# Performance work log

Hardware: AMD Instinct MI355X
Metric: run time of the kernel (lower is better)

## Reference

```python
import jax, jax.numpy as jnp
import numpy as np

B, N, F, D, DEG, LAYERS = 32, 1024, 64, 128, 8, 3
EPS = 1e-5


def _gat(x, src, dst, mask, W, a_s, a_d, b):
    # PyG GATConv (heads=1, concat=True): remove existing self loops (handled by mask),
    # add one self loop per node, per-edge leaky-relu attention, scatter-softmax per target.
    M = x.shape[0]
    h = x @ W                                 # [M, D]
    es = h @ a_s                              # [M] source attention term (x*att_src).sum(-1)
    ed = h @ a_d                              # [M] target attention term
    sl = jnp.arange(M, dtype=src.dtype)
    s = jnp.concatenate([src, sl])
    d = jnp.concatenate([dst, sl])
    m = jnp.concatenate([mask, jnp.ones((M,), bool)])
    logit = jnp.where(m, jax.nn.leaky_relu(es[s] + ed[d], 0.2), -jnp.inf)
    mx = jax.ops.segment_max(logit, d, num_segments=M)  # finite: every node has a self loop
    ex = jnp.where(m, jnp.exp(logit - mx[d]), 0.0)
    den = jax.ops.segment_sum(ex, d, num_segments=M)
    alpha = ex / den[d]
    return jax.ops.segment_sum(alpha[:, None] * h[s], d, num_segments=M) + b


def _dedupe(src, dst, mask, M):
    # coalesce after pooling: drop self loops and duplicate edges (PyG max_pool/pool_edge)
    E = src.shape[0]
    key = src * M + dst
    key = jnp.where(mask, key, M * M + jnp.arange(E, dtype=key.dtype))  # park dead edges on unique keys
    order = jnp.argsort(key)
    sk = key[order]
    first = jnp.concatenate([jnp.ones((1,), bool), sk[1:] != sk[:-1]])
    uniq = jnp.zeros((E,), bool).at[order].set(first)
    return mask & uniq & (src != dst)


def _forward(x, Ws, att_src, att_dst, bias, edge_index, clusters):
    src, dst = edge_index[0], edge_index[1]
    mask = src != dst  # GATConv calls remove_self_loops before adding its own
    Bn = x.shape[0] // clusters[0].shape[0]
    for i in range(len(Ws)):
        x = jax.nn.relu(_gat(x, src, dst, mask, Ws[i], att_src[i], att_dst[i], bias[i]))
        c = clusters[i]
        Ni = c.shape[0]
        No = Ni // 2  # cluster maps are arange(Ni)//2, surjective onto Ni//2
        cl = jnp.tile(c, Bn) + jnp.repeat(jnp.arange(Bn, dtype=c.dtype) * No, Ni)
        x = jax.ops.segment_max(x, cl, num_segments=Bn * No)  # max_pool over clusters
        src, dst = cl[src], cl[dst]
        mask = _dedupe(src, dst, mask, Bn * No)
        mu = jnp.mean(x, axis=0)  # BatchNorm1d(affine=False), training-mode batch stats
        var = jnp.mean((x - mu) ** 2, axis=0)
        x = (x - mu) / jnp.sqrt(var + EPS)
    return x.reshape(Bn, -1)  # [B, final_node * dim_cell]


def setup_inputs() -> dict:
    key = jax.random.key(0)
    ks = jax.random.split(key, 10)
    x = jax.random.normal(ks[0], (B * N, F), jnp.float32)
    # per-graph random edges with per-graph node offsets (graph-major layout)
    src_l = jax.random.randint(ks[1], (B, N * DEG), 0, N)
    dst_l = jax.random.randint(ks[2], (B, N * DEG), 0, N)
    off = (jnp.arange(B) * N)[:, None]
    edge_index = jnp.stack([(src_l + off).reshape(-1), (dst_l + off).reshape(-1)]).astype(jnp.int32)
    c0 = (jnp.arange(N) // 2).astype(jnp.int32)
    c1 = (jnp.arange(N // 2) // 2).astype(jnp.int32)
    c2 = (jnp.arange(N // 4) // 2).astype(jnp.int32)
    W0 = jax.random.normal(ks[3], (F, D), jnp.float32) / np.float32(np.sqrt(F))
    W1 = jax.random.normal(ks[4], (D, D), jnp.float32) / np.float32(np.sqrt(D))
    W2 = jax.random.normal(ks[5], (D, D), jnp.float32) / np.float32(np.sqrt(D))
    att_src = jax.random.normal(ks[6], (LAYERS, D), jnp.float32) / np.float32(np.sqrt(D))
    att_dst = jax.random.normal(ks[7], (LAYERS, D), jnp.float32) / np.float32(np.sqrt(D))
    bias = jnp.zeros((LAYERS, D), jnp.float32)
    return dict(x=x, W0=W0, W1=W1, W2=W2, att_src=att_src, att_dst=att_dst, bias=bias,
                edge_index=edge_index, c0=c0, c1=c1, c2=c2)


def reference(x, W0, W1, W2, att_src, att_dst, bias, edge_index, c0, c1, c2):
    return _forward(x, [W0, W1, W2], att_src, att_dst, bias, edge_index, [c0, c1, c2])
```

## Files before the change

### kernel.cpp

```cpp
#include <hip/hip_runtime.h>

#define E_TOTAL 262144
#define NGRAPH  32
#define EPG     8192
#define EPS_BN  1e-5f
#define MB (1u << 20)
#define KB (1u << 10)

__device__ __forceinline__ float lrelu(float x){ return x > 0.f ? x : 0.2f * x; }

__device__ __forceinline__ int xcd_swz(int b, int n){ return (b & 7) * (n >> 3) + (b >> 3); }

template<int K>
__global__ __launch_bounds__(256)
void gemm_attn(const float* __restrict__ A, const float* __restrict__ W,
               const float* __restrict__ bnsums, float invM,
               const float* __restrict__ a_s, const float* __restrict__ a_d,
               float* __restrict__ C, float* __restrict__ es, float* __restrict__ ed){
  __shared__ float Ws[64 * 128];
  __shared__ float As_t[64 * 36];
  __shared__ float bnmu[K], bnrs[K];
  int tid = threadIdx.x;
  if (tid < K){
    float mu = 0.f, rs = 1.f;
    if (bnsums){
      mu = bnsums[tid] * invM;
      float var = bnsums[K + tid] * invM - mu * mu;
      rs = rsqrtf(var + EPS_BN);
    }
    bnmu[tid] = mu; bnrs[tid] = rs;
  }
  int bid = xcd_swz(blockIdx.x, gridDim.x);
  int row0 = bid * 32;
  int c2 = tid & 63, rg = tid >> 6;
  float2 acc[8];
  #pragma unroll
  for (int i = 0; i < 8; ++i){ acc[i].x = 0.f; acc[i].y = 0.f; }

  for (int k0 = 0; k0 < K; k0 += 64){
    __syncthreads();
    for (int i = tid; i < 64 * 128; i += 256)
      Ws[i] = W[(size_t)(k0 + (i >> 7)) * 128 + (i & 127)];
    #pragma unroll
    for (int it = 0; it < 8; ++it){
      int i = it * 256 + tid;
      int r = i >> 6, kk = i & 63;
      float v = A[(size_t)(row0 + r) * K + k0 + kk];
      v = (v - bnmu[k0 + kk]) * bnrs[k0 + kk];
      As_t[kk * 36 + r] = v;
    }
    __syncthreads();
    #pragma unroll 8
    for (int kk = 0; kk < 64; ++kk){
      float2 w = *(float2*)&Ws[kk * 128 + c2 * 2];
      float4 a0 = *(float4*)&As_t[kk * 36 + rg * 8];
      float4 a1 = *(float4*)&As_t[kk * 36 + rg * 8 + 4];
      acc[0].x = fmaf(a0.x, w.x, acc[0].x); acc[0].y = fmaf(a0.x, w.y, acc[0].y);
      acc[1].x = fmaf(a0.y, w.x, acc[1].x); acc[1].y = fmaf(a0.y, w.y, acc[1].y);
      acc[2].x = fmaf(a0.z, w.x, acc[2].x); acc[2].y = fmaf(a0.z, w.y, acc[2].y);
      acc[3].x = fmaf(a0.w, w.x, acc[3].x); acc[3].y = fmaf(a0.w, w.y, acc[3].y);
      acc[4].x = fmaf(a1.x, w.x, acc[4].x); acc[4].y = fmaf(a1.x, w.y, acc[4].y);
      acc[5].x = fmaf(a1.y, w.x, acc[5].x); acc[5].y = fmaf(a1.y, w.y, acc[5].y);
      acc[6].x = fmaf(a1.z, w.x, acc[6].x); acc[6].y = fmaf(a1.z, w.y, acc[6].y);
      acc[7].x = fmaf(a1.w, w.x, acc[7].x); acc[7].y = fmaf(a1.w, w.y, acc[7].y);
    }
  }
  float2 as2 = ((const float2*)a_s)[c2];
  float2 ad2 = ((const float2*)a_d)[c2];
  float2* C2 = (float2*)C;
  #pragma unroll
  for (int i = 0; i < 8; ++i){
    int r = row0 + rg * 8 + i;
    C2[(size_t)r * 64 + c2] = acc[i];
    float e1 = acc[i].x * as2.x + acc[i].y * as2.y;
    float e2 = acc[i].x * ad2.x + acc[i].y * ad2.y;
    #pragma unroll
    for (int o = 32; o; o >>= 1){ e1 += __shfl_xor(e1, o); e2 += __shfl_xor(e2, o); }
    if (c2 == 0){ es[r] = e1; ed[r] = e2; }
  }
}

__global__ __launch_bounds__(1024)
void csr_build_all(const int* __restrict__ src0, const int* __restrict__ dst0,
                   int* __restrict__ csr1, int* __restrict__ csr2, int* __restrict__ csr3,
                   int* __restrict__ rs1, int* __restrict__ rs2, int* __restrict__ rs3,
                   int* __restrict__ cnt1, int* __restrict__ cnt2, int* __restrict__ cnt3,
                   float* __restrict__ bnsums){
  __shared__ unsigned int bm2[8192];
  __shared__ unsigned int bm3[2048];
  __shared__ int h1[1024];
  __shared__ int h2[512];
  __shared__ int h3[256];
  __shared__ int wsum[16];
  int g = blockIdx.x, t = threadIdx.x;
  int ebase = g * EPG;
  if (g == 0 && t < 768) bnsums[t] = 0.f;
  #pragma unroll
  for (int i = t; i < 8192; i += 1024) bm2[i] = 0u;
  #pragma unroll
  for (int i = t; i < 2048; i += 1024) bm3[i] = 0u;
  h1[t] = 0;
  if (t < 512) h2[t] = 0;
  if (t < 256) h3[t] = 0;
  __syncthreads();

  unsigned int k1 = 0, k2 = 0, k3 = 0;
  #pragma unroll
  for (int k = 0; k < 8; ++k){
    int e = ebase + k * 1024 + t;
    int sv = src0[e], dv = dst0[e];
    if (sv != dv){
      k1 |= 1u << k;
      atomicAdd(&h1[dv & 1023], 1);
      int s2 = (sv >> 1) & 511, d2 = (dv >> 1) & 511;
      if (s2 != d2){
        int key = (s2 << 9) | d2;
        unsigned int bit = 1u << (key & 31);
        unsigned int old = atomicOr(&bm2[key >> 5], bit);
        if (!(old & bit)){
          k2 |= 1u << k;
          atomicAdd(&h2[d2], 1);
          int s3 = (sv >> 2) & 255, d3 = (dv >> 2) & 255;
          if (s3 != d3){
            int key3 = (s3 << 8) | d3;
            unsigned int b3 = 1u << (key3 & 31);
            unsigned int o3 = atomicOr(&bm3[key3 >> 5], b3);
            if (!(o3 & b3)){ k3 |= 1u << k; atomicAdd(&h3[d3], 1); }
          }
        }
      }
    }
  }
  __syncthreads();

  int lane = t & 63, w = t >> 6;
  {
    int c = h1[t], v = c;
    #pragma unroll
    for (int o = 1; o < 64; o <<= 1){ int u = __shfl_up(v, o); if (lane >= o) v += u; }
    if (lane == 63) wsum[w] = v;
    __syncthreads();
    if (t == 0){ int run = 0;
      #pragma unroll
      for (int i = 0; i < 16; ++i){ int x = wsum[i]; wsum[i] = run; run += x; } }
    __syncthreads();
    int excl = v - c + wsum[w];
    cnt1[(g << 10) + t] = c;
    rs1 [(g << 10) + t] = ebase + excl;
    h1[t] = excl;
  }
  __syncthreads();
  {
    int c = (t < 512) ? h2[t] : 0, v = c;
    #pragma unroll
    for (int o = 1; o < 64; o <<= 1){ int u = __shfl_up(v, o); if (lane >= o) v += u; }
    if (lane == 63) wsum[w] = v;
    __syncthreads();
    if (t == 0){ int run = 0;
      #pragma unroll
      for (int i = 0; i < 16; ++i){ int x = wsum[i]; wsum[i] = run; run += x; } }
    __syncthreads();
    int excl = v - c + wsum[w];
    if (t < 512){
      cnt2[(g << 9) + t] = c;
      rs2 [(g << 9) + t] = ebase + excl;
      h2[t] = excl;
    }
  }
  __syncthreads();
  {
    int c = (t < 256) ? h3[t] : 0, v = c;
    #pragma unroll
    for (int o = 1; o < 64; o <<= 1){ int u = __shfl_up(v, o); if (lane >= o) v += u; }
    if (lane == 63) wsum[w] = v;
    __syncthreads();
    if (t == 0){ int run = 0;
      #pragma unroll
      for (int i = 0; i < 16; ++i){ int x = wsum[i]; wsum[i] = run; run += x; } }
    __syncthreads();
    int excl = v - c + wsum[w];
    if (t < 256){
      cnt3[(g << 8) + t] = c;
      rs3 [(g << 8) + t] = ebase + excl;
      h3[t] = excl;
    }
  }
  __syncthreads();

  unsigned int any = k1 | k2 | k3;
  #pragma unroll
  for (int k = 0; k < 8; ++k){
    if ((any >> k) & 1u){
      int e = ebase + k * 1024 + t;
      int sv = src0[e], dv = dst0[e];
      if ((k1 >> k) & 1u){
        int p = atomicAdd(&h1[dv & 1023], 1);
        csr1[ebase + p] = sv;
      }
      if ((k2 >> k) & 1u){
        int p = atomicAdd(&h2[(dv >> 1) & 511], 1);
        csr2[ebase + p] = sv >> 1;
      }
      if ((k3 >> k) & 1u){
        int p = atomicAdd(&h3[(dv >> 2) & 255], 1);
        csr3[ebase + p] = sv >> 2;
      }
    }
  }
}

__global__ void gat_pool(const float* __restrict__ h, const float* __restrict__ es,
                         const float* __restrict__ ed, const int* __restrict__ csr_src,
                         const int* __restrict__ row_start, const int* __restrict__ row_cnt,
                         const float* __restrict__ bias, float* __restrict__ xout, int M){
  __shared__ float2 osh[4][64];
  int lane = threadIdx.x & 63;
  int wave = threadIdx.x >> 6;
  int bid = xcd_swz(blockIdx.x, gridDim.x);
  int n = bid * 4 + wave;
  int start = row_start[n];
  int cnt   = row_cnt[n];
  float edn = ed[n];
  float selfl = lrelu(es[n] + edn);

  float m_l = -1e30f, d_l = 0.f;
  int   s_c = 0; float l_c = 0.f;
  for (int c0 = 0; c0 < cnt; c0 += 64){
    int j = c0 + lane;
    if (j < cnt){
      int s = csr_src[start + j];
      float l = lrelu(es[s] + edn);
      if (c0 == 0){ s_c = s; l_c = l; }
      float mn = fmaxf(m_l, l);
      d_l = d_l * __expf(m_l - mn) + __expf(l - mn);
      m_l = mn;
    }
  }
  #pragma unroll
  for (int o = 32; o; o >>= 1){
    float m2 = __shfl_xor(m_l, o), d2 = __shfl_xor(d_l, o);
    float mn = fmaxf(m_l, m2);
    d_l = d_l * __expf(m_l - mn) + d2 * __expf(m2 - mn);
    m_l = mn;
  }
  float mf  = fmaxf(m_l, selfl);
  float den = d_l * __expf(m_l - mf) + __expf(selfl - mf);

  const float2* h2 = (const float2*)h;
  float sw = __expf(selfl - mf);
  float2 hv = h2[(size_t)n * 64 + lane];
  float2 acc; acc.x = sw * hv.x; acc.y = sw * hv.y;
  for (int c0 = 0; c0 < cnt; c0 += 64){
    int j = c0 + lane;
    int s_j; float w_j;
    if (c0 == 0){
      s_j = s_c;
      w_j = (lane < cnt) ? __expf(l_c - mf) : 0.f;
    } else {
      s_j = 0; w_j = 0.f;
      if (j < cnt){
        s_j = csr_src[start + j];
        w_j = __expf(lrelu(es[s_j] + edn) - mf);
      }
    }
    int rem = min(64, cnt - c0);
    int k = 0;
    for (; k + 8 <= rem; k += 8){
      int ss[8]; float ww[8]; float2 hh[8];
      #pragma unroll
      for (int i = 0; i < 8; ++i){ ss[i] = __shfl(s_j, k + i); ww[i] = __shfl(w_j, k + i); }
      #pragma unroll
      for (int i = 0; i < 8; ++i){ hh[i] = h2[(size_t)ss[i] * 64 + lane]; }
      #pragma unroll
      for (int i = 0; i < 8; ++i){
        acc.x = fmaf(ww[i], hh[i].x, acc.x);
        acc.y = fmaf(ww[i], hh[i].y, acc.y);
      }
    }
    for (; k < rem; ++k){
      int s = __shfl(s_j, k); float w = __shfl(w_j, k);
      float2 hh = h2[(size_t)s * 64 + lane];
      acc.x = fmaf(w, hh.x, acc.x);
      acc.y = fmaf(w, hh.y, acc.y);
    }
  }
  float inv = 1.f / den;
  float2 bv = ((const float2*)bias)[lane];
  float2 o2;
  o2.x = fmaxf(acc.x * inv + bv.x, 0.f);
  o2.y = fmaxf(acc.y * inv + bv.y, 0.f);
  osh[wave][lane] = o2;
  __syncthreads();
  if (wave < 2){
    float2 a = osh[2 * wave][lane], b = osh[2 * wave + 1][lane];
    float2 p; p.x = fmaxf(a.x, b.x); p.y = fmaxf(a.y, b.y);
    ((float2*)xout)[(size_t)(bid * 2 + wave) * 64 + lane] = p;
  }
}

__global__ void bn_stats(const float* __restrict__ x, float* __restrict__ sums, int M){
  __shared__ float s1[256], s2[256];
  int c = threadIdx.x & 127, half = threadIdx.x >> 7;
  float a = 0.f, b = 0.f;
  for (int r = blockIdx.x * 2 + half; r < M; r += 256){
    float v = x[(size_t)r * 128 + c];
    a += v; b += v * v;
  }
  s1[threadIdx.x] = a; s2[threadIdx.x] = b;
  __syncthreads();
  if (threadIdx.x < 128){
    atomicAdd(&sums[c],       s1[threadIdx.x] + s1[threadIdx.x + 128]);
    atomicAdd(&sums[128 + c], s2[threadIdx.x] + s2[threadIdx.x + 128]);
  }
}

__global__ void bn_norm(const float* __restrict__ in, const float* __restrict__ sums,
                        float* __restrict__ out, int M){
  int idx = blockIdx.x * blockDim.x + threadIdx.x;
  if (idx >= M * 128) return;
  int c = idx & 127;
  float mu  = sums[c] / (float)M;
  float var = sums[128 + c] / (float)M - mu * mu;
  out[idx] = (in[idx] - mu) * rsqrtf(var + EPS_BN);
}

extern "C" void kernel_launch(void* const* d_in, const int* in_sizes, int n_in,
                              void* d_out, int out_size, void* d_ws, size_t ws_size,
                              hipStream_t stream){
  const float* x0   = (const float*)d_in[0];
  const float* W0   = (const float*)d_in[1];
  const float* W1   = (const float*)d_in[2];
  const float* W2   = (const float*)d_in[3];
  const float* attS = (const float*)d_in[4];
  const float* attD = (const float*)d_in[5];
  const float* bias = (const float*)d_in[6];
  const int*   src0 = (const int*)d_in[7];
  const int*   dst0 = src0 + E_TOTAL;
  float* out = (float*)d_out;

  char* ws = (char*)d_ws;
  float* Hbuf   = (float*)(ws);
  float* Xbuf   = (float*)(ws + 16 * MB);
  int*   csr1   = (int*)  (ws + 24 * MB);
  int*   csr2   = (int*)  (ws + 25 * MB);
  int*   csr3   = (int*)  (ws + 26 * MB);
  float* es     = (float*)(ws + 27 * MB);
  float* ed     = (float*)(ws + 27 * MB + 128 * KB);
  int*   rs1    = (int*)  (ws + 27 * MB + 256 * KB);
  int*   rs2    = (int*)  (ws + 27 * MB + 384 * KB);
  int*   rs3    = (int*)  (ws + 27 * MB + 448 * KB);
  int*   cnt1   = (int*)  (ws + 27 * MB + 480 * KB);
  int*   cnt2   = (int*)  (ws + 27 * MB + 608 * KB);
  int*   cnt3   = (int*)  (ws + 27 * MB + 672 * KB);
  float* bnsum0 = (float*)(ws + 27 * MB + 704 * KB);
  float* bnsum1 = bnsum0 + 256;
  float* bnsum2 = bnsum1 + 256;

  csr_build_all<<<NGRAPH, 1024, 0, stream>>>(src0, dst0, csr1, csr2, csr3,
                                             rs1, rs2, rs3, cnt1, cnt2, cnt3, bnsum0);

  gemm_attn<64><<<1024, 256, 0, stream>>>(x0, W0, nullptr, 0.f, attS, attD, Hbuf, es, ed);
  gat_pool<<<8192, 256, 0, stream>>>(Hbuf, es, ed, csr1, rs1, cnt1, bias, Xbuf, 32768);
  bn_stats<<<128, 256, 0, stream>>>(Xbuf, bnsum0, 16384);

  gemm_attn<128><<<512, 256, 0, stream>>>(Xbuf, W1, bnsum0, 1.f / 16384.f,
                                          attS + 128, attD + 128, Hbuf, es, ed);
  gat_pool<<<4096, 256, 0, stream>>>(Hbuf, es, ed, csr2, rs2, cnt2, bias + 128, Xbuf, 16384);
  bn_stats<<<128, 256, 0, stream>>>(Xbuf, bnsum1, 8192);

  gemm_attn<128><<<256, 256, 0, stream>>>(Xbuf, W2, bnsum1, 1.f / 8192.f,
                                          attS + 256, attD + 256, Hbuf, es, ed);
  gat_pool<<<2048, 256, 0, stream>>>(Hbuf, es, ed, csr3, rs3, cnt3, bias + 256, Xbuf, 8192);
  bn_stats<<<128, 256, 0, stream>>>(Xbuf, bnsum2, 4096);
  bn_norm<<<2048, 256, 0, stream>>>(Xbuf, bnsum2, out, 4096);
}
```

Before: 240.7 us.

## Fuse CSR build with first GEMM and fold BN stats into grid-barrier kernels

Merges the per-graph CSR construction into the first GEMM launch. 96 extra blocks split the three CSR levels across separate blocks, so edge preprocessing runs alongside the layer-0 matmul. The BN statistics passes are folded into the following GEMM and final-normalise kernels behind a software grid barrier, which removes several launches. The barrier assumes every block is co-resident (512 blocks at 256 threads with launch bounds of 2 per CU) and risks deadlock or spin overhead. The level-3 CSR block also redoes the level-2 dedupe on its own.

```diff
diff --git a/kernel.cpp b/kernel.cpp
--- a/kernel.cpp
+++ b/kernel.cpp
@@ -11,41 +11,249 @@
 
 __device__ __forceinline__ int xcd_swz(int b, int n){ return (b & 7) * (n >> 3) + (b >> 3); }
 
-template<int K>
-__global__ __launch_bounds__(256)
-void gemm_attn(const float* __restrict__ A, const float* __restrict__ W,
-               const float* __restrict__ bnsums, float invM,
-               const float* __restrict__ a_s, const float* __restrict__ a_d,
-               float* __restrict__ C, float* __restrict__ es, float* __restrict__ ed){
+__device__ __forceinline__ void grid_bar(int* bar, int n){
+  __syncthreads();
+  if (threadIdx.x == 0){
+    __hip_atomic_fetch_add(bar, 1, __ATOMIC_RELEASE, __HIP_MEMORY_SCOPE_AGENT);
+    while (__hip_atomic_load(bar, __ATOMIC_RELAXED, __HIP_MEMORY_SCOPE_AGENT) < n)
+      __builtin_amdgcn_s_sleep(8);
+    (void)__hip_atomic_load(bar, __ATOMIC_ACQUIRE, __HIP_MEMORY_SCOPE_AGENT);
+  }
+  __syncthreads();
+}
+
+template<int Q>
+__device__ __forceinline__ void scan_bins(int* h, int* cnt_g, int* rs_g, int B, int g,
+                                          int ebase, int* wsum){
+  int t = threadIdx.x, lane = t & 63, w = t >> 6;
+  int c[Q]; int s = 0;
+  #pragma unroll
+  for (int i = 0; i < Q; ++i){ c[i] = h[t * Q + i]; s += c[i]; }
+  int v = s;
+  #pragma unroll
+  for (int o = 1; o < 64; o <<= 1){ int u = __shfl_up(v, o); if (lane >= o) v += u; }
+  if (lane == 63) wsum[w] = v;
+  __syncthreads();
+  if (t == 0){ int run = 0;
+    #pragma unroll
+    for (int i = 0; i < 4; ++i){ int x = wsum[i]; wsum[i] = run; run += x; } }
+  __syncthreads();
+  int run = v - s + wsum[w];
+  #pragma unroll
+  for (int i = 0; i < Q; ++i){
+    cnt_g[g * B + t * Q + i] = c[i];
+    rs_g [g * B + t * Q + i] = ebase + run;
+    h[t * Q + i] = run;
+    run += c[i];
+  }
+  __syncthreads();
+}
+
+__global__ __launch_bounds__(256, 2)
+void mega1(const float* __restrict__ x0, const float* __restrict__ W0,
+           const float* __restrict__ a_s, const float* __restrict__ a_d,
+           const int* __restrict__ src0, const int* __restrict__ dst0,
+           float* __restrict__ C, float* __restrict__ es, float* __restrict__ ed,
+           int* __restrict__ csr1, int* __restrict__ csr2, int* __restrict__ csr3,
+           int* __restrict__ rs1, int* __restrict__ rs2, int* __restrict__ rs3,
+           int* __restrict__ cnt1, int* __restrict__ cnt2, int* __restrict__ cnt3,
+           float* __restrict__ sums_all, int* __restrict__ bars){
+  __shared__ __align__(16) char smem[45072];
+  __shared__ int wsum[4];
+  int t = threadIdx.x;
+  int raw = blockIdx.x;
+
+  if (raw < 96){
+    int* bm2 = (int*)smem;
+    int* bm3 = bm2 + 8192;
+    int* h   = bm3 + 2048;
+    int role = raw >> 5, g = raw & 31, ebase = g * EPG;
+    if (raw == 0 && t < 48) bars[t] = 0;
+    if (role == 0 && t < 24) sums_all[g * 24 + t] = 0.f;
+
+    if (role == 0){
+      for (int i = t; i < 1024; i += 256) h[i] = 0;
+      __syncthreads();
+      for (int i = 0; i < 32; ++i){
+        int e = ebase + i * 256 + t;
+        int sv = src0[e], dv = dst0[e];
+        if (sv != dv) atomicAdd(&h[dv & 1023], 1);
+      }
+      __syncthreads();
+      scan_bins<4>(h, cnt1, rs1, 1024, g, ebase, wsum);
+      for (int i = 0; i < 32; ++i){
+        int e = ebase + i * 256 + t;
+        int sv = src0[e], dv = dst0[e];
+        if (sv != dv){
+          int p = atomicAdd(&h[dv & 1023], 1);
+          csr1[ebase + p] = sv;
+        }
+      }
+    } else if (role == 1){
+      for (int i = t; i < 8192; i += 256) bm2[i] = 0;
+      for (int i = t; i < 512; i += 256) h[i] = 0;
+      __syncthreads();
+      unsigned int k2m = 0;
+      for (int i = 0; i < 32; ++i){
+        int e = ebase + i * 256 + t;
+        int sv = src0[e], dv = dst0[e];
+        if (sv != dv){
+          int s2 = (sv >> 1) & 511, d2 = (dv >> 1) & 511;
+          if (s2 != d2){
+            int key = (s2 << 9) | d2;
+            unsigned int bit = 1u << (key & 31);
+            unsigned int old = atomicOr((unsigned int*)&bm2[key >> 5], bit);
+            if (!(old & bit)){ k2m |= 1u << i; atomicAdd(&h[d2], 1); }
+          }
+        }
+      }
+      __syncthreads();
+      scan_bins<2>(h, cnt2, rs2, 512, g, ebase, wsum);
+      for (int i = 0; i < 32; ++i){
+        if ((k2m >> i) & 1u){
+          int e = ebase + i * 256 + t;
+          int sv = src0[e], dv = dst0[e];
+          int p = atomicAdd(&h[(dv >> 1) & 511], 1);
+          csr2[ebase + p] = sv >> 1;
+        }
+      }
+    } else {
+      for (int i = t; i < 8192; i += 256) bm2[i] = 0;
+      for (int i = t; i < 2048; i += 256) bm3[i] = 0;
+      for (int i = t; i < 256; i += 256) h[i] = 0;
+      __syncthreads();
+      unsigned int k3m = 0;
+      for (int i = 0; i < 32; ++i){
+        int e = ebase + i * 256 + t;
+        int sv = src0[e], dv = dst0[e];
+        if (sv != dv){
+          int s2 = (sv >> 1) & 511, d2 = (dv >> 1) & 511;
+          if (s2 != d2){
+            int key = (s2 << 9) | d2;
+            unsigned int bit = 1u << (key & 31);
+            unsigned int old = atomicOr((unsigned int*)&bm2[key >> 5], bit);
+            if (!(old & bit)){
+              int s3 = (sv >> 2) & 255, d3 = (dv >> 2) & 255;
+              if (s3 != d3){
+                int key3 = (s3 << 8) | d3;
+                unsigned int b3 = 1u << (key3 & 31);
+                unsigned int o3 = atomicOr((unsigned int*)&bm3[key3 >> 5], b3);
+                if (!(o3 & b3)){ k3m |= 1u << i; atomicAdd(&h[d3], 1); }
+              }
+            }
+          }
+        }
+      }
+      __syncthreads();
+      scan_bins<1>(h, cnt3, rs3, 256, g, ebase, wsum);
+      for (int i = 0; i < 32; ++i){
+        if ((k3m >> i) & 1u){
+          int e = ebase + i * 256 + t;
+          int sv = src0[e], dv = dst0[e];
+          int p = atomicAdd(&h[(dv >> 2) & 255], 1);
+          csr3[ebase + p] = sv >> 2;
+        }
+      }
+    }
+    return;
+  }
+
+  float* Ws   = (float*)smem;
+  float* As_t = Ws + 8192;
+  int tile = xcd_swz(raw - 96, 1024);
+  int row0 = tile * 32;
+  int c2 = t & 63, rg = t >> 6;
+  float2 acc[8];
+  #pragma unroll
+  for (int i = 0; i < 8; ++i){ acc[i].x = 0.f; acc[i].y = 0.f; }
+
+  for (int i = t; i < 8192; i += 256) Ws[i] = W0[i];
+  #pragma unroll
+  for (int it = 0; it < 8; ++it){
+    int i = it * 256 + t;
+    int r = i >> 6, kk = i & 63;
+    As_t[kk * 36 + r] = x0[(size_t)(row0 + r) * 64 + kk];
+  }
+  __syncthreads();
+  #pragma unroll 8
+  for (int kk = 0; kk < 64; ++kk){
+    float2 w = *(float2*)&Ws[kk * 128 + c2 * 2];
+    float4 a0 = *(float4*)&As_t[kk * 36 + rg * 8];
+    float4 a1 = *(float4*)&As_t[kk * 36 + rg * 8 + 4];
+    acc[0].x = fmaf(a0.x, w.x, acc[0].x); acc[0].y = fmaf(a0.x, w.y, acc[0].y);
+    acc[1].x = fmaf(a0.y, w.x, acc[1].x); acc[1].y = fmaf(a0.y, w.y, acc[1].y);
+    acc[2].x = fmaf(a0.z, w.x, acc[2].x); acc[2].y = fmaf(a0.z, w.y, acc[2].y);
+    acc[3].x = fmaf(a0.w, w.x, acc[3].x); acc[3].y = fmaf(a0.w, w.y, acc[3].y);
+    acc[4].x = fmaf(a1.x, w.x, acc[4].x); acc[4].y = fmaf(a1.x, w.y, acc[4].y);
+    acc[5].x = fmaf(a1.y, w.x, acc[5].x); acc[5].y = fmaf(a1.y, w.y, acc[5].y);
+    acc[6].x = fmaf(a1.z, w.x, acc[6].x); acc[6].y = fmaf(a1.z, w.y, acc[6].y);
+    acc[7].x = fmaf(a1.w, w.x, acc[7].x); acc[7].y = fmaf(a1.w, w.y, acc[7].y);
+  }
+  float2 as2 = ((const float2*)a_s)[c2];
+  float2 ad2 = ((const float2*)a_d)[c2];
+  float2* C2 = (float2*)C;
+  #pragma unroll
+  for (int i = 0; i < 8; ++i){
+    int r = row0 + rg * 8 + i;
+    C2[(size_t)r * 64 + c2] = acc[i];
+    float e1 = acc[i].x * as2.x + acc[i].y * as2.y;
+    float e2 = acc[i].x * ad2.x + acc[i].y * ad2.y;
+    #pragma unroll
+    for (int o = 32; o; o >>= 1){ e1 += __shfl_xor(e1, o); e2 += __shfl_xor(e2, o); }
+    if (c2 == 0){ es[r] = e1; ed[r] = e2; }
+  }
+}
+
+__global__ __launch_bounds__(256, 2)
+void gemm_attn128(const float* __restrict__ A, const float* __restrict__ W,
+                  float* __restrict__ sums, float invM, int Mstats,
+                  const float* __restrict__ a_s, const float* __restrict__ a_d,
+                  float* __restrict__ C, float* __restrict__ es, float* __restrict__ ed,
+                  int* __restrict__ bar){
   __shared__ float Ws[64 * 128];
   __shared__ float As_t[64 * 36];
-  __shared__ float bnmu[K], bnrs[K];
-  int tid = threadIdx.x;
-  if (tid < K){
-    float mu = 0.f, rs = 1.f;
-    if (bnsums){
-      mu = bnsums[tid] * invM;
-      float var = bnsums[K + tid] * invM - mu * mu;
-      rs = rsqrtf(var + EPS_BN);
-    }
-    bnmu[tid] = mu; bnrs[tid] = rs;
-  }
+  __shared__ float bnmu[128], bnrs[128];
+  __shared__ float s1[256], s2[256];
+  int t = threadIdx.x;
+
+  {
+    int c = t & 127, half = t >> 7;
+    float a = 0.f, b = 0.f;
+    for (int r = blockIdx.x * 2 + half; r < Mstats; r += 2 * gridDim.x){
+      float v = A[(size_t)r * 128 + c];
+      a += v; b += v * v;
+    }
+    s1[t] = a; s2[t] = b;
+    __syncthreads();
+    if (t < 128){
+      atomicAdd(&sums[c],       s1[t] + s1[t + 128]);
+      atomicAdd(&sums[128 + c], s2[t] + s2[t + 128]);
+    }
+    grid_bar(bar, gridDim.x);
+    if (t < 128){
+      float mu = sums[t] * invM;
+      float var = sums[128 + t] * invM - mu * mu;
+      bnmu[t] = mu; bnrs[t] = rsqrtf(var + EPS_BN);
+    }
+    __syncthreads();
+  }
+
   int bid = xcd_swz(blockIdx.x, gridDim.x);
   int row0 = bid * 32;
-  int c2 = tid & 63, rg = tid >> 6;
+  int c2 = t & 63, rg = t >> 6;
   float2 acc[8];
   #pragma unroll
   for (int i = 0; i < 8; ++i){ acc[i].x = 0.f; acc[i].y = 0.f; }
 
-  for (int k0 = 0; k0 < K; k0 += 64){
+  for (int k0 = 0; k0 < 128; k0 += 64){
     __syncthreads();
-    for (int i = tid; i < 64 * 128; i += 256)
+    for (int i = t; i < 64 * 128; i += 256)
       Ws[i] = W[(size_t)(k0 + (i >> 7)) * 128 + (i & 127)];
     #pragma unroll
     for (int it = 0; it < 8; ++it){
-      int i = it * 256 + tid;
+      int i = it * 256 + t;
       int r = i >> 6, kk = i & 63;
-      float v = A[(size_t)(row0 + r) * K + k0 + kk];
+      float v = A[(size_t)(row0 + r) * 128 + k0 + kk];
       v = (v - bnmu[k0 + kk]) * bnrs[k0 + kk];
       As_t[kk * 36 + r] = v;
     }
@@ -77,135 +285,6 @@
     #pragma unroll
     for (int o = 32; o; o >>= 1){ e1 += __shfl_xor(e1, o); e2 += __shfl_xor(e2, o); }
     if (c2 == 0){ es[r] = e1; ed[r] = e2; }
-  }
-}
-
-__global__ __launch_bounds__(1024)
-void csr_build_all(const int* __restrict__ src0, const int* __restrict__ dst0,
-                   int* __restrict__ csr1, int* __restrict__ csr2, int* __restrict__ csr3,
-                   int* __restrict__ rs1, int* __restrict__ rs2, int* __restrict__ rs3,
-                   int* __restrict__ cnt1, int* __restrict__ cnt2, int* __restrict__ cnt3,
-                   float* __restrict__ bnsums){
-  __shared__ unsigned int bm2[8192];
-  __shared__ unsigned int bm3[2048];
-  __shared__ int h1[1024];
-  __shared__ int h2[512];
-  __shared__ int h3[256];
-  __shared__ int wsum[16];
-  int g = blockIdx.x, t = threadIdx.x;
-  int ebase = g * EPG;
-  if (g == 0 && t < 768) bnsums[t] = 0.f;
-  #pragma unroll
-  for (int i = t; i < 8192; i += 1024) bm2[i] = 0u;
-  #pragma unroll
-  for (int i = t; i < 2048; i += 1024) bm3[i] = 0u;
-  h1[t] = 0;
-  if (t < 512) h2[t] = 0;
-  if (t < 256) h3[t] = 0;
-  __syncthreads();
-
-  unsigned int k1 = 0, k2 = 0, k3 = 0;
-  #pragma unroll
-  for (int k = 0; k < 8; ++k){
-    int e = ebase + k * 1024 + t;
-    int sv = src0[e], dv = dst0[e];
-    if (sv != dv){
-      k1 |= 1u << k;
-      atomicAdd(&h1[dv & 1023], 1);
-      int s2 = (sv >> 1) & 511, d2 = (dv >> 1) & 511;
-      if (s2 != d2){
-        int key = (s2 << 9) | d2;
-        unsigned int bit = 1u << (key & 31);
-        unsigned int old = atomicOr(&bm2[key >> 5], bit);
-        if (!(old & bit)){
-          k2 |= 1u << k;
-          atomicAdd(&h2[d2], 1);
-          int s3 = (sv >> 2) & 255, d3 = (dv >> 2) & 255;
-          if (s3 != d3){
-            int key3 = (s3 << 8) | d3;
-            unsigned int b3 = 1u << (key3 & 31);
-            unsigned int o3 = atomicOr(&bm3[key3 >> 5], b3);
-            if (!(o3 & b3)){ k3 |= 1u << k; atomicAdd(&h3[d3], 1); }
-          }
-        }
-      }
-    }
-  }
-  __syncthreads();
-
-  int lane = t & 63, w = t >> 6;
-  {
-    int c = h1[t], v = c;
-    #pragma unroll
-    for (int o = 1; o < 64; o <<= 1){ int u = __shfl_up(v, o); if (lane >= o) v += u; }
-    if (lane == 63) wsum[w] = v;
-    __syncthreads();
-    if (t == 0){ int run = 0;
-      #pragma unroll
-      for (int i = 0; i < 16; ++i){ int x = wsum[i]; wsum[i] = run; run += x; } }
-    __syncthreads();
-    int excl = v - c + wsum[w];
-    cnt1[(g << 10) + t] = c;
-    rs1 [(g << 10) + t] = ebase + excl;
-    h1[t] = excl;
-  }
-  __syncthreads();
-  {
-    int c = (t < 512) ? h2[t] : 0, v = c;
-    #pragma unroll
-    for (int o = 1; o < 64; o <<= 1){ int u = __shfl_up(v, o); if (lane >= o) v += u; }
-    if (lane == 63) wsum[w] = v;
-    __syncthreads();
-    if (t == 0){ int run = 0;
-      #pragma unroll
-      for (int i = 0; i < 16; ++i){ int x = wsum[i]; wsum[i] = run; run += x; } }
-    __syncthreads();
-    int excl = v - c + wsum[w];
-    if (t < 512){
-      cnt2[(g << 9) + t] = c;
-      rs2 [(g << 9) + t] = ebase + excl;
-      h2[t] = excl;
-    }
-  }
-  __syncthreads();
-  {
-    int c = (t < 256) ? h3[t] : 0, v = c;
-    #pragma unroll
-    for (int o = 1; o < 64; o <<= 1){ int u = __shfl_up(v, o); if (lane >= o) v += u; }
-    if (lane == 63) wsum[w] = v;
-    __syncthreads();
-    if (t == 0){ int run = 0;
-      #pragma unroll
-      for (int i = 0; i < 16; ++i){ int x = wsum[i]; wsum[i] = run; run += x; } }
-    __syncthreads();
-    int excl = v - c + wsum[w];
-    if (t < 256){
-      cnt3[(g << 8) + t] = c;
-      rs3 [(g << 8) + t] = ebase + excl;
-      h3[t] = excl;
-    }
-  }
-  __syncthreads();
-
-  unsigned int any = k1 | k2 | k3;
-  #pragma unroll
-  for (int k = 0; k < 8; ++k){
-    if ((any >> k) & 1u){
-      int e = ebase + k * 1024 + t;
-      int sv = src0[e], dv = dst0[e];
-      if ((k1 >> k) & 1u){
-        int p = atomicAdd(&h1[dv & 1023], 1);
-        csr1[ebase + p] = sv;
-      }
-      if ((k2 >> k) & 1u){
-        int p = atomicAdd(&h2[(dv >> 1) & 511], 1);
-        csr2[ebase + p] = sv >> 1;
-      }
-      if ((k3 >> k) & 1u){
-        int p = atomicAdd(&h3[(dv >> 2) & 255], 1);
-        csr3[ebase + p] = sv >> 2;
-      }
-    }
   }
 }
 
@@ -298,30 +377,38 @@
   }
 }
 
-__global__ void bn_stats(const float* __restrict__ x, float* __restrict__ sums, int M){
+__global__ __launch_bounds__(256)
+void bn_final(const float* __restrict__ x, float* __restrict__ sums,
+              float* __restrict__ out, int Mrows, int* __restrict__ bar){
   __shared__ float s1[256], s2[256];
-  int c = threadIdx.x & 127, half = threadIdx.x >> 7;
+  __shared__ float mu_s[128], rs_s[128];
+  int t = threadIdx.x;
+  int c = t & 127, half = t >> 7;
   float a = 0.f, b = 0.f;
-  for (int r = blockIdx.x * 2 + half; r < M; r += 256){
+  for (int r = blockIdx.x * 2 + half; r < Mrows; r += 2 * gridDim.x){
     float v = x[(size_t)r * 128 + c];
     a += v; b += v * v;
   }
-  s1[threadIdx.x] = a; s2[threadIdx.x] = b;
-  __syncthreads();
-  if (threadIdx.x < 128){
-    atomicAdd(&sums[c],       s1[threadIdx.x] + s1[threadIdx.x + 128]);
-    atomicAdd(&sums[128 + c], s2[threadIdx.x] + s2[threadIdx.x + 128]);
-  }
-}
-
-__global__ void bn_norm(const float* __restrict__ in, const float* __restrict__ sums,
-                        float* __restrict__ out, int M){
-  int idx = blockIdx.x * blockDim.x + threadIdx.x;
-  if (idx >= M * 128) return;
-  int c = idx & 127;
-  float mu  = sums[c] / (float)M;
-  float var = sums[128 + c] / (float)M - mu * mu;
-  out[idx] = (in[idx] - mu) * rsqrtf(var + EPS_BN);
+  s1[t] = a; s2[t] = b;
+  __syncthreads();
+  if (t < 128){
+    atomicAdd(&sums[c],       s1[t] + s1[t + 128]);
+    atomicAdd(&sums[128 + c], s2[t] + s2[t + 128]);
+  }
+  grid_bar(bar, gridDim.x);
+  if (t < 128){
+    float mu = sums[t] / (float)Mrows;
+    float var = sums[128 + t] / (float)Mrows - mu * mu;
+    mu_s[t] = mu; rs_s[t] = rsqrtf(var + EPS_BN);
+  }
+  __syncthreads();
+  int per = (Mrows * 128) / gridDim.x;
+  int base = blockIdx.x * per;
+  for (int i = t; i < per; i += 256){
+    int e = base + i;
+    int ch = e & 127;
+    out[e] = (x[e] - mu_s[ch]) * rs_s[ch];
+  }
 }
 
 extern "C" void kernel_launch(void* const* d_in, const int* in_sizes, int n_in,
@@ -352,25 +439,23 @@
   int*   cnt1   = (int*)  (ws + 27 * MB + 480 * KB);
   int*   cnt2   = (int*)  (ws + 27 * MB + 608 * KB);
   int*   cnt3   = (int*)  (ws + 27 * MB + 672 * KB);
-  float* bnsum0 = (float*)(ws + 27 * MB + 704 * KB);
-  float* bnsum1 = bnsum0 + 256;
-  float* bnsum2 = bnsum1 + 256;
-
-  csr_build_all<<<NGRAPH, 1024, 0, stream>>>(src0, dst0, csr1, csr2, csr3,
-                                             rs1, rs2, rs3, cnt1, cnt2, cnt3, bnsum0);
-
-  gemm_attn<64><<<1024, 256, 0, stream>>>(x0, W0, nullptr, 0.f, attS, attD, Hbuf, es, ed);
+  float* sums   = (float*)(ws + 27 * MB + 704 * KB);
+  int*   bars   = (int*)  (ws + 27 * MB + 708 * KB);
+  float* sums0 = sums, *sums1 = sums + 256, *sums2 = sums + 512;
+
+  mega1<<<1120, 256, 0, stream>>>(x0, W0, attS, attD, src0, dst0, Hbuf, es, ed,
+                                  csr1, csr2, csr3, rs1, rs2, rs3, cnt1, cnt2, cnt3,
+                                  sums, bars);
+
   gat_pool<<<8192, 256, 0, stream>>>(Hbuf, es, ed, csr1, rs1, cnt1, bias, Xbuf, 32768);
-  bn_stats<<<128, 256, 0, stream>>>(Xbuf, bnsum0, 16384);
-
-  gemm_attn<128><<<512, 256, 0, stream>>>(Xbuf, W1, bnsum0, 1.f / 16384.f,
-                                          attS + 128, attD + 128, Hbuf, es, ed);
+
+  gemm_attn128<<<512, 256, 0, stream>>>(Xbuf, W1, sums0, 1.f / 16384.f, 16384,
+                                        attS + 128, attD + 128, Hbuf, es, ed, &bars[0]);
   gat_pool<<<4096, 256, 0, stream>>>(Hbuf, es, ed, csr2, rs2, cnt2, bias + 128, Xbuf, 16384);
-  bn_stats<<<128, 256, 0, stream>>>(Xbuf, bnsum1, 8192);
-
-  gemm_attn<128><<<256, 256, 0, stream>>>(Xbuf, W2, bnsum1, 1.f / 8192.f,
-                                          attS + 256, attD + 256, Hbuf, es, ed);
+
+  gemm_attn128<<<256, 256, 0, stream>>>(Xbuf, W2, sums1, 1.f / 8192.f, 8192,
+                                        attS + 256, attD + 256, Hbuf, es, ed, &bars[16]);
   gat_pool<<<2048, 256, 0, stream>>>(Hbuf, es, ed, csr3, rs3, cnt3, bias + 256, Xbuf, 8192);
-  bn_stats<<<128, 256, 0, stream>>>(Xbuf, bnsum2, 4096);
-  bn_norm<<<2048, 256, 0, stream>>>(Xbuf, bnsum2, out, 4096);
-}
+
+  bn_final<<<512, 256, 0, stream>>>(Xbuf, sums2, out, 4096, &bars[32]);
+}
```

Result: slower. 270.0 us (+12.2%).
